# Kernel optimization log

Measured on AMD Instinct MI355X. Metric: run time of the kernel, lower is better.

Reference implementation:

```python
import jax, jax.numpy as jnp
import numpy as np

LN_EPS = 1e-5

def _layernorm(x, g, b):
    m = jnp.mean(x, axis=-1, keepdims=True)
    v = jnp.var(x, axis=-1, keepdims=True)
    return (x - m) * jax.lax.rsqrt(v + LN_EPS) * g + b

def setup_inputs() -> dict:
    key = jax.random.key(0)
    ks = jax.random.split(key, 12)
    BT, D, OH, OW = 32, 768, 28, 43
    N, NFB, NFC = 12, 1024, 256
    s = 0.02
    return {
        "roi_feature": jax.random.normal(ks[0], (BT * N, NFB), jnp.float32),
        "image_feature": jax.random.normal(ks[1], (BT, D, OH, OW), jnp.float32),
        "conv_w": jax.random.normal(ks[2], (NFC, D), jnp.float32) * s,
        "conv_b": jnp.zeros((NFC,), jnp.float32),
        "emb_w": jax.random.normal(ks[3], (NFC, NFB), jnp.float32) * s,
        "emb_b": jnp.zeros((NFC,), jnp.float32),
        "ln1_g": jnp.ones((NFC,), jnp.float32),
        "ln1_b": jnp.zeros((NFC,), jnp.float32),
        "ffn_w1": jax.random.normal(ks[4], (NFC, NFC), jnp.float32) * s,
        "ffn_b1": jnp.zeros((NFC,), jnp.float32),
        "ffn_w2": jax.random.normal(ks[5], (NFC, NFC), jnp.float32) * s,
        "ffn_b2": jnp.zeros((NFC,), jnp.float32),
        "ln2_g": jnp.ones((NFC,), jnp.float32),
        "ln2_b": jnp.zeros((NFC,), jnp.float32),
        "N": 12,
        "layer_id": 1,
    }

def reference(roi_feature, image_feature, conv_w, conv_b, emb_w, emb_b,
              ln1_g, ln1_b, ffn_w1, ffn_b1, ffn_w2, ffn_b2, ln2_g, ln2_b,
              N, layer_id):
    BT, D, OH, OW = image_feature.shape
    NFC = conv_w.shape[0]
    # 1x1 conv == channel GEMM: [BT, D, OH, OW] -> [BT, NFC, OH*OW]
    img = jnp.einsum('bchw,oc->bohw', image_feature, conv_w) + conv_b[None, :, None, None]
    img = img.reshape(BT, NFC, OH * OW)                       # [BT, NFC, P]
    # roi embedding: [BT*N, NFB] -> [BT, N, NFC]
    emb = (roi_feature @ emb_w.T + emb_b).reshape(BT, N, NFC)
    # cross-attention: logits [BT, N, P], softmax over spatial positions
    logits = jnp.einsum('bnc,bcp->bnp', emb, img)
    A = jax.nn.softmax(logits, axis=2)
    ctx = jnp.einsum('bnp,bcp->bnc', A, img).reshape(BT * N, NFC)
    # residual + LN1 (dropout is identity at inference)
    x = _layernorm(ctx + emb.reshape(BT * N, NFC), ln1_g, ln1_b)
    # FFN residual + LN2
    h = jax.nn.relu(x @ ffn_w1.T + ffn_b1) @ ffn_w2.T + ffn_b2
    return _layernorm(x + h, ln2_g, ln2_b)
```

## Files before the change

### kernel.cpp

```cpp
#include <hip/hip_runtime.h>
#include <hip/hip_bf16.h>
#include <stdint.h>

typedef __hip_bfloat16 bf16;
typedef __attribute__((ext_vector_type(8))) __bf16 frag8;
typedef __attribute__((ext_vector_type(4))) float f32x4;

#define GLDS16(gsrc, ldst)                                                        \
  __builtin_amdgcn_global_load_lds(                                               \
      (const __attribute__((address_space(1))) void*)(gsrc),                      \
      (__attribute__((address_space(3))) void*)(ldst), 16, 0, 0)

__device__ inline float wred_sum(float v) {
#pragma unroll
  for (int o = 32; o; o >>= 1) v += __shfl_down(v, o);
  return v;
}
__device__ inline float wred_max(float v) {
#pragma unroll
  for (int o = 32; o; o >>= 1) v = fmaxf(v, __shfl_down(v, o));
  return v;
}
__device__ inline unsigned short bits_of(bf16 h) { return *(unsigned short*)&h; }

__global__ __launch_bounds__(256) void convert_all(
    const float* __restrict__ s0, bf16* __restrict__ d0, int n0,
    const float* __restrict__ s1, bf16* __restrict__ d1, int n1,
    const float* __restrict__ s2, bf16* __restrict__ d2, int n2,
    const float* __restrict__ s3, bf16* __restrict__ d3, int n3,
    const float* __restrict__ s4, bf16* __restrict__ d4, int n4) {
  int i = blockIdx.x * 256 + threadIdx.x;
  if (i < n0) { d0[i] = __float2bfloat16(s0[i]); return; } i -= n0;
  if (i < n1) { d1[i] = __float2bfloat16(s1[i]); return; } i -= n1;
  if (i < n2) { d2[i] = __float2bfloat16(s2[i]); return; } i -= n2;
  if (i < n3) { d3[i] = __float2bfloat16(s3[i]); return; } i -= n3;
  if (i < n4) { d4[i] = __float2bfloat16(s4[i]); }
}

__global__ __launch_bounds__(512) void conv_fused(
    const float* __restrict__ X, const bf16* __restrict__ W,
    const float* __restrict__ bias, bf16* __restrict__ img) {
  int b = blockIdx.y;
  int p0 = blockIdx.x * 128;
  __shared__ __align__(16) bf16 lA[256 * 32];
  __shared__ __align__(16) bf16 lB[128 * 32];
  int tid = threadIdx.x, w = tid >> 6, lane = tid & 63;
  int wm = w >> 1, wn = w & 1;
  int lr = lane & 15, kg = lane >> 4;
  int sc = (tid >> 5) * 2;
  int spq = (tid & 31) * 4;
  const int prem = 1204 - p0;
  f32x4 acc[4][4] = {};
  for (int k0 = 0; k0 < 768; k0 += 32) {
#pragma unroll
    for (int i = 0; i < 2; ++i) {
      int off = w * 1024 + i * 8192 + lane * 16;
      int row = off >> 6, kb = off & 63;
      GLDS16((const char*)W + (long)row * 1536 + k0 * 2 + kb,
             (char*)lA + w * 1024 + i * 8192);
    }
    const float* xr = X + ((long)b * 768 + k0 + sc) * 1204 + p0 + spq;
    float v0[4], v1[4];
    if (prem >= 128) {
      float4 a0 = *(const float4*)xr;
      float4 a1 = *(const float4*)(xr + 1204);
      v0[0] = a0.x; v0[1] = a0.y; v0[2] = a0.z; v0[3] = a0.w;
      v1[0] = a1.x; v1[1] = a1.y; v1[2] = a1.z; v1[3] = a1.w;
    } else {
#pragma unroll
      for (int j = 0; j < 4; ++j) {
        bool ok = (spq + j) < prem;
        v0[j] = ok ? xr[j] : 0.f;
        v1[j] = ok ? xr[1204 + j] : 0.f;
      }
    }
#pragma unroll
    for (int j = 0; j < 4; ++j) {
      int p = spq + j;
      unsigned pk = (unsigned)bits_of(__float2bfloat16(v0[j]))
                  | ((unsigned)bits_of(__float2bfloat16(v1[j])) << 16);
      int byte = (p << 6) + sc * 2;
      byte ^= ((p >> 3) & 7) << 4;
      *(unsigned*)((char*)lB + byte) = pk;
    }
    __syncthreads();
    frag8 af[4], bv[4];
#pragma unroll
    for (int mi = 0; mi < 4; ++mi)
      af[mi] = *(const frag8*)((const char*)lA + (wm * 64 + mi * 16 + lr) * 64 + kg * 16);
#pragma unroll
    for (int ni = 0; ni < 4; ++ni) {
      int pl = wn * 64 + ni * 16 + lr;
      int byte = (pl << 6) + kg * 16;
      byte ^= ((pl >> 3) & 7) << 4;
      bv[ni] = *(const frag8*)((const char*)lB + byte);
    }
#pragma unroll
    for (int mi = 0; mi < 4; ++mi)
#pragma unroll
      for (int ni = 0; ni < 4; ++ni)
        acc[mi][ni] = __builtin_amdgcn_mfma_f32_16x16x32_bf16(af[mi], bv[ni], acc[mi][ni], 0, 0, 0);
    __syncthreads();
  }
#pragma unroll
  for (int mi = 0; mi < 4; ++mi)
#pragma unroll
    for (int ni = 0; ni < 4; ++ni)
#pragma unroll
      for (int j = 0; j < 4; ++j) {
        int o = wm * 64 + mi * 16 + kg * 4 + j;
        int p = p0 + wn * 64 + ni * 16 + lr;
        float v = acc[mi][ni][j] + bias[o];
        img[((long)b * 256 + o) * 1280 + p] = __float2bfloat16(v);
      }
}

template <bool BIAS_ROW, bool RELU, bool OUT_BF16>
__global__ __launch_bounds__(256) void gemm_tn(
    const bf16* __restrict__ A, long sA, const bf16* __restrict__ B, long sB,
    void* __restrict__ C, long sC, int K, int ldc, const float* __restrict__ bias) {
  int bz = blockIdx.z;
  int n0 = blockIdx.x * 128, m0 = blockIdx.y * 128;
  const bf16* Ab = A + bz * sA + (long)m0 * K;
  const bf16* Bb = B + bz * sB + (long)n0 * K;
  __shared__ __align__(16) bf16 lA[128 * 32];
  __shared__ __align__(16) bf16 lB[128 * 32];
  int tid = threadIdx.x;
  int w = tid >> 6, lane = tid & 63;
  int wm = w >> 1, wn = w & 1;
  int lr = lane & 15, kg = lane >> 4;
  f32x4 acc[4][4] = {};
  for (int k0 = 0; k0 < K; k0 += 32) {
#pragma unroll
    for (int i = 0; i < 2; ++i) {
      int off = w * 2048 + i * 1024 + lane * 16;
      int row = off >> 6, kb = off & 63;
      long gbyte = (long)row * (K * 2) + (long)k0 * 2 + kb;
      GLDS16((const char*)Ab + gbyte, (char*)lA + w * 2048 + i * 1024);
      GLDS16((const char*)Bb + gbyte, (char*)lB + w * 2048 + i * 1024);
    }
    __syncthreads();
    frag8 af[4], bv[4];
#pragma unroll
    for (int mi = 0; mi < 4; ++mi)
      af[mi] = *(const frag8*)((const char*)lA + (wm * 64 + mi * 16 + lr) * 64 + kg * 16);
#pragma unroll
    for (int ni = 0; ni < 4; ++ni)
      bv[ni] = *(const frag8*)((const char*)lB + (wn * 64 + ni * 16 + lr) * 64 + kg * 16);
#pragma unroll
    for (int mi = 0; mi < 4; ++mi)
#pragma unroll
      for (int ni = 0; ni < 4; ++ni)
        acc[mi][ni] = __builtin_amdgcn_mfma_f32_16x16x32_bf16(af[mi], bv[ni], acc[mi][ni], 0, 0, 0);
    __syncthreads();
  }
#pragma unroll
  for (int mi = 0; mi < 4; ++mi)
#pragma unroll
    for (int ni = 0; ni < 4; ++ni)
#pragma unroll
      for (int j = 0; j < 4; ++j) {
        int row = m0 + wm * 64 + mi * 16 + kg * 4 + j;
        int col = n0 + wn * 64 + ni * 16 + lr;
        float v = acc[mi][ni][j];
        v += BIAS_ROW ? bias[row] : bias[col];
        if (RELU) v = fmaxf(v, 0.f);
        long idx = (long)bz * sC + (long)row * ldc + col;
        if constexpr (OUT_BF16) ((bf16*)C)[idx] = __float2bfloat16(v);
        else ((float*)C)[idx] = v;
      }
}

__global__ __launch_bounds__(256) void logits_k(const bf16* __restrict__ img,
                                                const float* __restrict__ emb,
                                                float* __restrict__ lgt) {
  int b = blockIdx.x;
  __shared__ float e[3072];
  const float* eb = emb + (long)b * 3072;
  for (int i = threadIdx.x; i < 3072; i += 256) e[i] = eb[i];
  __syncthreads();
  int p = blockIdx.y * 256 + threadIdx.x;
  if (p >= 1204) return;
  const bf16* ib = img + (long)b * 256 * 1280 + p;
  float acc[12] = {};
#pragma unroll 4
  for (int c = 0; c < 256; ++c) {
    float xv = __bfloat162float(ib[(long)c * 1280]);
#pragma unroll
    for (int n = 0; n < 12; ++n) acc[n] += e[n * 256 + c] * xv;
  }
#pragma unroll
  for (int n = 0; n < 12; ++n) lgt[((long)b * 12 + n) * 1204 + p] = acc[n];
}

__global__ __launch_bounds__(256) void softmax_k(const float* __restrict__ lgt,
                                                 bf16* __restrict__ am) {
  int b = blockIdx.x, n = blockIdx.y, tid = threadIdx.x;
  bf16* row = am + ((long)b * 16 + n) * 1280;
  if (n >= 12) {
    for (int i = tid; i < 1280; i += 256) row[i] = __float2bfloat16(0.f);
    return;
  }
  const float* lr = lgt + ((long)b * 12 + n) * 1204;
  float vals[5];
  float m = -3.0e38f;
#pragma unroll
  for (int i = 0; i < 5; ++i) {
    int pp = tid + i * 256;
    vals[i] = (pp < 1204) ? lr[pp] : -3.0e38f;
    m = fmaxf(m, vals[i]);
  }
  m = wred_max(m);
  __shared__ float rd[4];
  int w = tid >> 6, lane = tid & 63;
  if (lane == 0) rd[w] = m;
  __syncthreads();
  m = fmaxf(fmaxf(rd[0], rd[1]), fmaxf(rd[2], rd[3]));
  float s = 0.f;
#pragma unroll
  for (int i = 0; i < 5; ++i) {
    int pp = tid + i * 256;
    vals[i] = (pp < 1204) ? __expf(vals[i] - m) : 0.f;
    s += vals[i];
  }
  s = wred_sum(s);
  __syncthreads();
  if (lane == 0) rd[w] = s;
  __syncthreads();
  s = rd[0] + rd[1] + rd[2] + rd[3];
  float inv = 1.f / s;
#pragma unroll
  for (int i = 0; i < 5; ++i) {
    int pp = tid + i * 256;
    row[pp] = __float2bfloat16((pp < 1204) ? vals[i] * inv : 0.f);
  }
}

__global__ __launch_bounds__(256) void ctx_split(const bf16* __restrict__ img,
                                                 const bf16* __restrict__ am,
                                                 float* __restrict__ cpart) {
  int b = blockIdx.x, kc = blockIdx.y;
  const bf16* Ab = img + (long)b * 256 * 1280;
  const bf16* Bb = am + (long)b * 16 * 1280;
  __shared__ __align__(16) bf16 lA[256 * 32];
  __shared__ __align__(16) bf16 lB[16 * 32];
  int tid = threadIdx.x, w = tid >> 6, lane = tid & 63;
  int lr = lane & 15, kg = lane >> 4;
  f32x4 acc[4] = {};
  int kend = kc * 256 + 256;
  for (int k0 = kc * 256; k0 < kend; k0 += 32) {
#pragma unroll
    for (int i = 0; i < 4; ++i) {
      int off = w * 4096 + i * 1024 + lane * 16;
      int row = off >> 6, kb = off & 63;
      GLDS16((const char*)Ab + (long)row * 2560 + k0 * 2 + kb,
             (char*)lA + w * 4096 + i * 1024);
    }
    if (w == 0) {
      int off = lane * 16, row = off >> 6, kb = off & 63;
      GLDS16((const char*)Bb + (long)row * 2560 + k0 * 2 + kb, (char*)lB);
    }
    __syncthreads();
    frag8 bv = *(const frag8*)((const char*)lB + lr * 64 + kg * 16);
#pragma unroll
    for (int mi = 0; mi < 4; ++mi) {
      frag8 av = *(const frag8*)((const char*)lA + (w * 64 + mi * 16 + lr) * 64 + kg * 16);
      acc[mi] = __builtin_amdgcn_mfma_f32_16x16x32_bf16(av, bv, acc[mi], 0, 0, 0);
    }
    __syncthreads();
  }
  int n = lr;
  if (n < 12) {
#pragma unroll
    for (int mi = 0; mi < 4; ++mi)
#pragma unroll
      for (int j = 0; j < 4; ++j)
        cpart[((long)kc * 384 + b * 12 + n) * 256 + (w * 64 + mi * 16 + kg * 4 + j)] =
            acc[mi][j];
  }
}

__global__ __launch_bounds__(256) void ln_k(const float* __restrict__ a, int nparts,
                                            long pstride, const float* __restrict__ bb,
                                            const float* __restrict__ g,
                                            const float* __restrict__ be,
                                            float* __restrict__ of,
                                            bf16* __restrict__ ob) {
  int r = blockIdx.x, c = threadIdx.x;
  long idx = (long)r * 256 + c;
  float v = bb[idx];
  for (int q = 0; q < nparts; ++q) v += a[idx + q * pstride];
  float s = wred_sum(v);
  float s2 = wred_sum(v * v);
  __shared__ float r1[4], r2[4];
  int w = c >> 6, lane = c & 63;
  if (lane == 0) { r1[w] = s; r2[w] = s2; }
  __syncthreads();
  float st = r1[0] + r1[1] + r1[2] + r1[3];
  float s2t = r2[0] + r2[1] + r2[2] + r2[3];
  float mean = st * (1.f / 256.f);
  float var = s2t * (1.f / 256.f) - mean * mean;
  float rs = rsqrtf(var + 1e-5f);
  float y = (v - mean) * rs * g[c] + be[c];
  if (of) of[idx] = y;
  if (ob) ob[idx] = __float2bfloat16(y);
}

extern "C" void kernel_launch(void* const* d_in, const int* in_sizes, int n_in,
                              void* d_out, int out_size, void* d_ws, size_t ws_size,
                              hipStream_t stream) {
  const float* roi   = (const float*)d_in[0];
  const float* imgf  = (const float*)d_in[1];
  const float* convw = (const float*)d_in[2];
  const float* convb = (const float*)d_in[3];
  const float* embw  = (const float*)d_in[4];
  const float* embb  = (const float*)d_in[5];
  const float* ln1g  = (const float*)d_in[6];
  const float* ln1b  = (const float*)d_in[7];
  const float* w1    = (const float*)d_in[8];
  const float* b1    = (const float*)d_in[9];
  const float* w2    = (const float*)d_in[10];
  const float* b2    = (const float*)d_in[11];
  const float* ln2g  = (const float*)d_in[12];
  const float* ln2b  = (const float*)d_in[13];
  float* out = (float*)d_out;

  char* p = (char*)d_ws;
  size_t off = 0;
  auto take = [&](size_t sz) -> char* {
    char* r = p + off;
    off += (sz + 255) & ~(size_t)255;
    return r;
  };
  bf16*  img   = (bf16*)take((size_t)32 * 256 * 1280 * 2);
  bf16*  cwb   = (bf16*)take((size_t)256 * 768 * 2);
  bf16*  ewb   = (bf16*)take((size_t)256 * 1024 * 2);
  bf16*  w1b   = (bf16*)take((size_t)256 * 256 * 2);
  bf16*  w2b   = (bf16*)take((size_t)256 * 256 * 2);
  bf16*  roib  = (bf16*)take((size_t)384 * 1024 * 2);
  float* emb   = (float*)take((size_t)384 * 256 * 4);
  float* lgt   = (float*)take((size_t)384 * 1204 * 4);
  bf16*  am    = (bf16*)take((size_t)32 * 16 * 1280 * 2);
  float* cpart = (float*)take((size_t)5 * 384 * 256 * 4);
  float* x     = (float*)take((size_t)384 * 256 * 4);
  bf16*  xb    = (bf16*)take((size_t)384 * 256 * 2);
  bf16*  h1    = (bf16*)take((size_t)384 * 256 * 2);
  float* h     = (float*)take((size_t)384 * 256 * 4);

  {
    int total = 196608 + 262144 + 65536 + 65536 + 393216;
    convert_all<<<(total + 255) / 256, 256, 0, stream>>>(
        convw, cwb, 196608, embw, ewb, 262144, w1, w1b, 65536, w2, w2b, 65536,
        roi, roib, 393216);
  }
  conv_fused<<<dim3(10, 32), 512, 0, stream>>>(imgf, cwb, convb, img);
  gemm_tn<false, false, false><<<dim3(2, 3, 1), 256, 0, stream>>>(
      roib, 0, ewb, 0, emb, 0, 1024, 256, embb);
  logits_k<<<dim3(32, 5), 256, 0, stream>>>(img, emb, lgt);
  softmax_k<<<dim3(32, 16), 256, 0, stream>>>(lgt, am);
  ctx_split<<<dim3(32, 5), 256, 0, stream>>>(img, am, cpart);
  ln_k<<<384, 256, 0, stream>>>(cpart, 5, (long)384 * 256, emb, ln1g, ln1b, x, xb);
  gemm_tn<false, true, true><<<dim3(2, 3, 1), 256, 0, stream>>>(
      xb, 0, w1b, 0, h1, 0, 256, 256, b1);
  gemm_tn<false, false, false><<<dim3(2, 3, 1), 256, 0, stream>>>(
      h1, 0, w2b, 0, h, 0, 256, 256, b2);
  ln_k<<<384, 256, 0, stream>>>(h, 1, 0, x, ln2g, ln2b, out, nullptr);
}
```

Baseline: 137.8 us.

## Double-buffer conv GEMM with register prefetch, smaller tiles; LDS-free small GEMMs

The 1x1-conv GEMM now uses 64-position tiles with 256 threads, which raises the block count from 320 to 608. Its K loop is double-buffered through registers so the next slice's global loads overlap MFMA work on the current LDS buffer, and the weight tile gets an XOR swizzle in LDS. The small embedding and FFN GEMMs are replaced by a single-wave 64x64 kernel that loads MFMA fragments straight from global memory, with no LDS or barriers, and uses 24 blocks instead of 6. This trades LDS data reuse for more parallelism and fewer synchronisations. The cost is extra global traffic and register pressure.

```diff
diff --git a/kernel.cpp b/kernel.cpp
--- a/kernel.cpp
+++ b/kernel.cpp
@@ -37,122 +37,132 @@
   if (i < n4) { d4[i] = __float2bfloat16(s4[i]); }
 }
 
-__global__ __launch_bounds__(512) void conv_fused(
+__global__ __launch_bounds__(256) void conv_fused(
     const float* __restrict__ X, const bf16* __restrict__ W,
     const float* __restrict__ bias, bf16* __restrict__ img) {
   int b = blockIdx.y;
-  int p0 = blockIdx.x * 128;
-  __shared__ __align__(16) bf16 lA[256 * 32];
-  __shared__ __align__(16) bf16 lB[128 * 32];
+  int p0 = blockIdx.x * 64;
+  __shared__ __align__(16) bf16 lA[2][256 * 32];
+  __shared__ __align__(16) bf16 lB[2][64 * 32];
   int tid = threadIdx.x, w = tid >> 6, lane = tid & 63;
-  int wm = w >> 1, wn = w & 1;
   int lr = lane & 15, kg = lane >> 4;
-  int sc = (tid >> 5) * 2;
-  int spq = (tid & 31) * 4;
-  const int prem = 1204 - p0;
+  int aro = tid >> 2, aslot = tid & 3;
+  int cpair = tid >> 4, pquad = tid & 15;
+  const bool edge = (p0 + 64 > 1204);
+
+  uint4 aR[4];
+  float bR0[4], bR1[4];
+
+  auto loadA = [&](int k0) {
+#pragma unroll
+    for (int q = 0; q < 4; ++q)
+      aR[q] = *(const uint4*)((const char*)W + (long)(q * 64 + aro) * 1536 +
+                              k0 * 2 + aslot * 16);
+  };
+  auto loadB = [&](int k0) {
+    const float* xb = X + ((long)b * 768 + k0 + 2 * cpair) * 1204 + p0 + pquad;
+    if (!edge) {
+#pragma unroll
+      for (int j = 0; j < 4; ++j) {
+        bR0[j] = xb[16 * j];
+        bR1[j] = xb[1204 + 16 * j];
+      }
+    } else {
+#pragma unroll
+      for (int j = 0; j < 4; ++j) {
+        bool ok = (p0 + pquad + 16 * j) < 1204;
+        bR0[j] = ok ? xb[16 * j] : 0.f;
+        bR1[j] = ok ? xb[1204 + 16 * j] : 0.f;
+      }
+    }
+  };
+  auto stage = [&](int buf) {
+    char* La = (char*)lA[buf];
+    char* Lb = (char*)lB[buf];
+#pragma unroll
+    for (int q = 0; q < 4; ++q) {
+      int o = q * 64 + aro;
+      int byte = (o * 64 + aslot * 16) ^ ((o & 7) << 4);
+      *(uint4*)(La + byte) = aR[q];
+    }
+#pragma unroll
+    for (int j = 0; j < 4; ++j) {
+      int p = pquad + 16 * j;
+      unsigned pk = (unsigned)bits_of(__float2bfloat16(bR0[j])) |
+                    ((unsigned)bits_of(__float2bfloat16(bR1[j])) << 16);
+      int byte = (p * 64 + cpair * 4) ^ ((p & 7) << 4);
+      *(unsigned*)(Lb + byte) = pk;
+    }
+  };
+
   f32x4 acc[4][4] = {};
-  for (int k0 = 0; k0 < 768; k0 += 32) {
-#pragma unroll
-    for (int i = 0; i < 2; ++i) {
-      int off = w * 1024 + i * 8192 + lane * 16;
-      int row = off >> 6, kb = off & 63;
-      GLDS16((const char*)W + (long)row * 1536 + k0 * 2 + kb,
-             (char*)lA + w * 1024 + i * 8192);
-    }
-    const float* xr = X + ((long)b * 768 + k0 + sc) * 1204 + p0 + spq;
-    float v0[4], v1[4];
-    if (prem >= 128) {
-      float4 a0 = *(const float4*)xr;
-      float4 a1 = *(const float4*)(xr + 1204);
-      v0[0] = a0.x; v0[1] = a0.y; v0[2] = a0.z; v0[3] = a0.w;
-      v1[0] = a1.x; v1[1] = a1.y; v1[2] = a1.z; v1[3] = a1.w;
-    } else {
+  loadA(0);
+  loadB(0);
+  for (int t = 0; t < 24; ++t) {
+    int buf = t & 1;
+    stage(buf);
+    if (t + 1 < 24) {
+      loadA((t + 1) * 32);
+      loadB((t + 1) * 32);
+    }
+    __syncthreads();
+    const char* La = (const char*)lA[buf];
+    const char* Lb = (const char*)lB[buf];
+    frag8 af[4], bv[4];
+#pragma unroll
+    for (int mi = 0; mi < 4; ++mi) {
+      int o = w * 64 + mi * 16 + lr;
+      af[mi] = *(const frag8*)(La + ((o * 64 + kg * 16) ^ ((o & 7) << 4)));
+    }
+#pragma unroll
+    for (int ni = 0; ni < 4; ++ni) {
+      int p = ni * 16 + lr;
+      bv[ni] = *(const frag8*)(Lb + ((p * 64 + kg * 16) ^ ((p & 7) << 4)));
+    }
+#pragma unroll
+    for (int mi = 0; mi < 4; ++mi)
+#pragma unroll
+      for (int ni = 0; ni < 4; ++ni)
+        acc[mi][ni] = __builtin_amdgcn_mfma_f32_16x16x32_bf16(af[mi], bv[ni],
+                                                              acc[mi][ni], 0, 0, 0);
+    __syncthreads();
+  }
+#pragma unroll
+  for (int mi = 0; mi < 4; ++mi)
+#pragma unroll
+    for (int ni = 0; ni < 4; ++ni)
 #pragma unroll
       for (int j = 0; j < 4; ++j) {
-        bool ok = (spq + j) < prem;
-        v0[j] = ok ? xr[j] : 0.f;
-        v1[j] = ok ? xr[1204 + j] : 0.f;
-      }
-    }
-#pragma unroll
-    for (int j = 0; j < 4; ++j) {
-      int p = spq + j;
-      unsigned pk = (unsigned)bits_of(__float2bfloat16(v0[j]))
-                  | ((unsigned)bits_of(__float2bfloat16(v1[j])) << 16);
-      int byte = (p << 6) + sc * 2;
-      byte ^= ((p >> 3) & 7) << 4;
-      *(unsigned*)((char*)lB + byte) = pk;
-    }
-    __syncthreads();
-    frag8 af[4], bv[4];
-#pragma unroll
-    for (int mi = 0; mi < 4; ++mi)
-      af[mi] = *(const frag8*)((const char*)lA + (wm * 64 + mi * 16 + lr) * 64 + kg * 16);
-#pragma unroll
-    for (int ni = 0; ni < 4; ++ni) {
-      int pl = wn * 64 + ni * 16 + lr;
-      int byte = (pl << 6) + kg * 16;
-      byte ^= ((pl >> 3) & 7) << 4;
-      bv[ni] = *(const frag8*)((const char*)lB + byte);
-    }
-#pragma unroll
-    for (int mi = 0; mi < 4; ++mi)
-#pragma unroll
-      for (int ni = 0; ni < 4; ++ni)
-        acc[mi][ni] = __builtin_amdgcn_mfma_f32_16x16x32_bf16(af[mi], bv[ni], acc[mi][ni], 0, 0, 0);
-    __syncthreads();
-  }
-#pragma unroll
-  for (int mi = 0; mi < 4; ++mi)
-#pragma unroll
-    for (int ni = 0; ni < 4; ++ni)
-#pragma unroll
-      for (int j = 0; j < 4; ++j) {
-        int o = wm * 64 + mi * 16 + kg * 4 + j;
-        int p = p0 + wn * 64 + ni * 16 + lr;
+        int o = w * 64 + mi * 16 + kg * 4 + j;
+        int p = p0 + ni * 16 + lr;
         float v = acc[mi][ni][j] + bias[o];
         img[((long)b * 256 + o) * 1280 + p] = __float2bfloat16(v);
       }
 }
 
-template <bool BIAS_ROW, bool RELU, bool OUT_BF16>
-__global__ __launch_bounds__(256) void gemm_tn(
-    const bf16* __restrict__ A, long sA, const bf16* __restrict__ B, long sB,
-    void* __restrict__ C, long sC, int K, int ldc, const float* __restrict__ bias) {
-  int bz = blockIdx.z;
-  int n0 = blockIdx.x * 128, m0 = blockIdx.y * 128;
-  const bf16* Ab = A + bz * sA + (long)m0 * K;
-  const bf16* Bb = B + bz * sB + (long)n0 * K;
-  __shared__ __align__(16) bf16 lA[128 * 32];
-  __shared__ __align__(16) bf16 lB[128 * 32];
-  int tid = threadIdx.x;
-  int w = tid >> 6, lane = tid & 63;
-  int wm = w >> 1, wn = w & 1;
-  int lr = lane & 15, kg = lane >> 4;
+template <bool RELU, bool OUT_BF16>
+__global__ __launch_bounds__(64) void gemm_sm(const bf16* __restrict__ A,
+                                              const bf16* __restrict__ B,
+                                              void* __restrict__ C, int K,
+                                              const float* __restrict__ bias) {
+  int n0 = blockIdx.x * 64, m0 = blockIdx.y * 64;
+  int lr = threadIdx.x & 15, kg = threadIdx.x >> 4;
   f32x4 acc[4][4] = {};
+#pragma unroll 2
   for (int k0 = 0; k0 < K; k0 += 32) {
-#pragma unroll
-    for (int i = 0; i < 2; ++i) {
-      int off = w * 2048 + i * 1024 + lane * 16;
-      int row = off >> 6, kb = off & 63;
-      long gbyte = (long)row * (K * 2) + (long)k0 * 2 + kb;
-      GLDS16((const char*)Ab + gbyte, (char*)lA + w * 2048 + i * 1024);
-      GLDS16((const char*)Bb + gbyte, (char*)lB + w * 2048 + i * 1024);
-    }
-    __syncthreads();
     frag8 af[4], bv[4];
 #pragma unroll
     for (int mi = 0; mi < 4; ++mi)
-      af[mi] = *(const frag8*)((const char*)lA + (wm * 64 + mi * 16 + lr) * 64 + kg * 16);
+      af[mi] = *(const frag8*)(A + (long)(m0 + mi * 16 + lr) * K + k0 + kg * 8);
 #pragma unroll
     for (int ni = 0; ni < 4; ++ni)
-      bv[ni] = *(const frag8*)((const char*)lB + (wn * 64 + ni * 16 + lr) * 64 + kg * 16);
+      bv[ni] = *(const frag8*)(B + (long)(n0 + ni * 16 + lr) * K + k0 + kg * 8);
 #pragma unroll
     for (int mi = 0; mi < 4; ++mi)
 #pragma unroll
       for (int ni = 0; ni < 4; ++ni)
-        acc[mi][ni] = __builtin_amdgcn_mfma_f32_16x16x32_bf16(af[mi], bv[ni], acc[mi][ni], 0, 0, 0);
-    __syncthreads();
+        acc[mi][ni] = __builtin_amdgcn_mfma_f32_16x16x32_bf16(af[mi], bv[ni],
+                                                              acc[mi][ni], 0, 0, 0);
   }
 #pragma unroll
   for (int mi = 0; mi < 4; ++mi)
@@ -160,12 +170,11 @@
     for (int ni = 0; ni < 4; ++ni)
 #pragma unroll
       for (int j = 0; j < 4; ++j) {
-        int row = m0 + wm * 64 + mi * 16 + kg * 4 + j;
-        int col = n0 + wn * 64 + ni * 16 + lr;
-        float v = acc[mi][ni][j];
-        v += BIAS_ROW ? bias[row] : bias[col];
+        int row = m0 + mi * 16 + kg * 4 + j;
+        int col = n0 + ni * 16 + lr;
+        float v = acc[mi][ni][j] + bias[col];
         if (RELU) v = fmaxf(v, 0.f);
-        long idx = (long)bz * sC + (long)row * ldc + col;
+        long idx = (long)row * 256 + col;
         if constexpr (OUT_BF16) ((bf16*)C)[idx] = __float2bfloat16(v);
         else ((float*)C)[idx] = v;
       }
@@ -353,16 +362,13 @@
         convw, cwb, 196608, embw, ewb, 262144, w1, w1b, 65536, w2, w2b, 65536,
         roi, roib, 393216);
   }
-  conv_fused<<<dim3(10, 32), 512, 0, stream>>>(imgf, cwb, convb, img);
-  gemm_tn<false, false, false><<<dim3(2, 3, 1), 256, 0, stream>>>(
-      roib, 0, ewb, 0, emb, 0, 1024, 256, embb);
+  gemm_sm<false, false><<<dim3(4, 6), 64, 0, stream>>>(roib, ewb, emb, 1024, embb);
+  conv_fused<<<dim3(19, 32), 256, 0, stream>>>(imgf, cwb, convb, img);
   logits_k<<<dim3(32, 5), 256, 0, stream>>>(img, emb, lgt);
   softmax_k<<<dim3(32, 16), 256, 0, stream>>>(lgt, am);
   ctx_split<<<dim3(32, 5), 256, 0, stream>>>(img, am, cpart);
   ln_k<<<384, 256, 0, stream>>>(cpart, 5, (long)384 * 256, emb, ln1g, ln1b, x, xb);
-  gemm_tn<false, true, true><<<dim3(2, 3, 1), 256, 0, stream>>>(
-      xb, 0, w1b, 0, h1, 0, 256, 256, b1);
-  gemm_tn<false, false, false><<<dim3(2, 3, 1), 256, 0, stream>>>(
-      h1, 0, w2b, 0, h, 0, 256, 256, b2);
+  gemm_sm<true, true><<<dim3(4, 6), 64, 0, stream>>>(xb, w1b, h1, 256, b1);
+  gemm_sm<false, false><<<dim3(4, 6), 64, 0, stream>>>(h1, w2b, h, 256, b2);
   ln_k<<<384, 256, 0, stream>>>(h, 1, 0, x, ln2g, ln2b, out, nullptr);
 }
```

Measured after the change: 186.6 us. +35.4%, slower.
